# Performance work log

Measured on AMD Instinct MI355X. Metric: run time of the kernel, lower is better.

Reference implementation:

```python
import jax, jax.numpy as jnp
import numpy as np

IN_C = 128
OUT_C = 128
KS = (5, 10, 15, 20)  # Chebyshev orders per filter (evenly spaced up to max_chebyshev_order=20)
NUM_FILTERS = len(KS)
LN_EPS = 1e-5


def setup_inputs() -> dict:
    key = jax.random.key(0)
    ks = jax.random.split(key, 10)
    N, E = 50000, 800000
    x = jax.random.normal(ks[0], (N, IN_C), dtype=jnp.float32)
    edge_index = jax.random.randint(ks[1], (2, E), 0, N, dtype=jnp.int64)
    total_K = sum(KS)
    cheb_w = jax.random.normal(ks[2], (total_K, IN_C, OUT_C), dtype=jnp.float32) * (1.0 / np.sqrt(IN_C))
    cheb_b = jax.random.normal(ks[3], (NUM_FILTERS, OUT_C), dtype=jnp.float32) * 0.01
    attn_w = jax.random.normal(ks[4], (NUM_FILTERS * OUT_C, NUM_FILTERS), dtype=jnp.float32) * (1.0 / np.sqrt(NUM_FILTERS * OUT_C))
    attn_b = jnp.zeros((NUM_FILTERS,), dtype=jnp.float32)
    ln_g = jnp.ones((OUT_C,), dtype=jnp.float32)
    ln_b = jnp.zeros((OUT_C,), dtype=jnp.float32)
    return {"x": x, "edge_index": edge_index, "cheb_w": cheb_w, "cheb_b": cheb_b,
            "attn_w": attn_w, "attn_b": attn_b, "ln_g": ln_g, "ln_b": ln_b}


def _scaled_laplacian(edge_index, N, dtype):
    # get_laplacian('sym'): L = I - D^{-1/2} A D^{-1/2}; then (2/lambda_max)*w - 1 with lambda_max=2
    row, col = edge_index[0], edge_index[1]
    w = jnp.ones(row.shape, dtype)
    deg = jax.ops.segment_sum(w, row, num_segments=N)
    dinv = jnp.where(deg > 0, jax.lax.rsqrt(jnp.maximum(deg, 1e-12)), 0.0).astype(dtype)
    lap_w = -dinv[row] * w * dinv[col]          # off-diagonal entries
    loop = jnp.arange(N, dtype=row.dtype)
    src = jnp.concatenate([row, loop])
    dst = jnp.concatenate([col, loop])
    lw = jnp.concatenate([lap_w, jnp.ones((N,), dtype)])  # diagonal = 1
    lw = (2.0 / 2.0) * lw - 1.0                 # faithful: -1 applied to EVERY stored entry
    return src, dst, lw


def _propagate(x, src, dst, w, N):
    # scatter-add of edge-weighted neighbor features (PyG propagate, aggr='add')
    return jax.ops.segment_sum(w[:, None] * x[src], dst, num_segments=N)


def _cheb_conv(x, src, dst, lw, W, b, K, N):
    Tx0 = x
    out = Tx0 @ W[0]
    if K > 1:
        Tx1 = _propagate(x, src, dst, lw, N)
        out = out + Tx1 @ W[1]
        for k in range(2, K):
            Tx2 = 2.0 * _propagate(Tx1, src, dst, lw, N) - Tx0
            out = out + Tx2 @ W[k]
            Tx0, Tx1 = Tx1, Tx2
    return out + b


def reference(x, edge_index, cheb_w, cheb_b, attn_w, attn_b, ln_g, ln_b):
    N = x.shape[0]
    src, dst, lw = _scaled_laplacian(edge_index, N, x.dtype)
    outs = []
    off = 0
    for i, K in enumerate(KS):
        W = cheb_w[off:off + K]
        outs.append(_cheb_conv(x, src, dst, lw, W, cheb_b[i], K, N))
        off += K
    stacked = jnp.stack(outs)                                  # [F, N, C]
    feats = jnp.concatenate(outs, axis=-1)                     # [N, F*C]
    attn = jax.nn.softmax(feats @ attn_w + attn_b, axis=-1)    # [N, F]
    combined = jnp.einsum('nf,fnc->nc', attn, stacked)         # [N, C]
    mu = jnp.mean(combined, axis=-1, keepdims=True)
    var = jnp.mean(jnp.square(combined - mu), axis=-1, keepdims=True)
    return (combined - mu) * jax.lax.rsqrt(var + LN_EPS) * ln_g + ln_b
```

## Files before the change

### kernel.cpp

```cpp
#include <hip/hip_runtime.h>

#define IN_C 128
#define NF 4

typedef __attribute__((ext_vector_type(8))) short short8;
typedef __attribute__((ext_vector_type(4))) float f32x4;

__device__ __forceinline__ unsigned short f2bf(float v) {
    unsigned u = __float_as_uint(v);
    return (unsigned short)((u + 0x7fffu + ((u >> 16) & 1u)) >> 16);
}

__global__ void zero_ints(int* p, int n) {
    int i = blockIdx.x * 256 + threadIdx.x;
    if (i < n) p[i] = 0;
}

__global__ void count_deg(const int* __restrict__ ei, int* __restrict__ degr,
                          int* __restrict__ cnt, int E) {
    int e = blockIdx.x * 256 + threadIdx.x;
    if (e >= E) return;
    atomicAdd(&degr[ei[e]], 1);
    atomicAdd(&cnt[ei[E + e]], 1);
}

__global__ void dinv_k(const int* __restrict__ degr, float* __restrict__ dinv, int N) {
    int i = blockIdx.x * 256 + threadIdx.x;
    if (i >= N) return;
    int d = degr[i];
    dinv[i] = (d > 0) ? rsqrtf((float)d) : 0.0f;
}

__global__ void scanA(const int* __restrict__ in, int* __restrict__ outp,
                      int* __restrict__ partials, int n) {
    __shared__ int tmp[256];
    int t = threadIdx.x;
    int gid = blockIdx.x * 256 + t;
    int v = (gid < n) ? in[gid] : 0;
    tmp[t] = v;
    __syncthreads();
    for (int off = 1; off < 256; off <<= 1) {
        int add = (t >= off) ? tmp[t - off] : 0;
        __syncthreads();
        tmp[t] += add;
        __syncthreads();
    }
    if (gid < n) outp[gid] = tmp[t] - v;
    if (t == 255) partials[blockIdx.x] = tmp[255];
}

__global__ void scanB(int* partials, int n) {
    __shared__ int tmp[256];
    int t = threadIdx.x;
    int v = (t < n) ? partials[t] : 0;
    tmp[t] = v;
    __syncthreads();
    for (int off = 1; off < 256; off <<= 1) {
        int add = (t >= off) ? tmp[t - off] : 0;
        __syncthreads();
        tmp[t] += add;
        __syncthreads();
    }
    if (t < n) partials[t] = tmp[t] - v;
}

__global__ void scanC(int* __restrict__ offs, const int* __restrict__ partials,
                      int n, int total) {
    int gid = blockIdx.x * 256 + threadIdx.x;
    if (gid < n) offs[gid] += partials[blockIdx.x];
    if (gid == 0) offs[n] = total;
}

__global__ void fill_csr(const int* __restrict__ ei, const float* __restrict__ dinv,
                         const int* __restrict__ offs, int* __restrict__ cursor,
                         uint2* __restrict__ csr, int E) {
    int e = blockIdx.x * 256 + threadIdx.x;
    if (e >= E) return;
    int r = ei[e];
    int c = ei[E + e];
    float w = -dinv[r] * dinv[c] - 1.0f;
    int pos = offs[c] + atomicAdd(&cursor[c], 1);
    csr[pos] = make_uint2((unsigned)r, __float_as_uint(w));
}

__global__ void wtr(const float* __restrict__ cheb_w, unsigned short* __restrict__ wht) {
    int gk = blockIdx.x;
    const float* src = cheb_w + (size_t)gk * 16384;
    unsigned short* dst = wht + (size_t)gk * 16384;
    for (int j = 0; j < 64; ++j) {
        int idx = threadIdx.x + j * 256;
        int c = idx >> 7, o = idx & 127;
        dst[o * 128 + c] = f2bf(src[idx]);
    }
}

__global__ void vprep(const float* __restrict__ cheb_w, const float* __restrict__ attn_w,
                      float* __restrict__ V) {
    int k = blockIdx.x;
    int c = threadIdx.x;
    float s[4] = {0.f, 0.f, 0.f, 0.f};
    for (int f = k / 5; f < 4; ++f) {
        const float* wrow = cheb_w + (size_t)((5 * f * (f + 1)) / 2 + k) * 16384 + c * 128;
        const float* arow = attn_w + (size_t)f * 512;
        for (int o = 0; o < 128; ++o) {
            float wv = wrow[o];
            s[0] += wv * arow[o * 4 + 0];
            s[1] += wv * arow[o * 4 + 1];
            s[2] += wv * arow[o * 4 + 2];
            s[3] += wv * arow[o * 4 + 3];
        }
    }
    float* dst = V + k * 512 + c * 4;
    dst[0] = s[0]; dst[1] = s[1]; dst[2] = s[2]; dst[3] = s[3];
}

__global__ void bias_const(const float* __restrict__ cheb_b, const float* __restrict__ attn_w,
                           const float* __restrict__ attn_b, float* __restrict__ constj) {
    int j = threadIdx.x;
    if (j >= 4) return;
    float s = attn_b[j];
    for (int t = 0; t < 512; ++t) s += cheb_b[t] * attn_w[t * 4 + j];
    constj[j] = s;
}

__global__ __launch_bounds__(256) void logit_init(
    const float* __restrict__ x, const float* __restrict__ V,
    const float* __restrict__ constj, float* __restrict__ logits,
    unsigned short* __restrict__ xb, int N)
{
    int node = blockIdx.x * 4 + (threadIdx.x >> 6);
    int lane = threadIdx.x & 63;
    if (node >= N) return;
    float2 v = ((const float2*)(x + (size_t)node * 128))[lane];
    int cc = lane * 2;
    unsigned u = (unsigned)f2bf(v.x) | ((unsigned)f2bf(v.y) << 16);
    *(unsigned*)(xb + (size_t)node * 128 + cc) = u;

    float4 va = *(const float4*)(V + 4 * cc);
    float4 vb = *(const float4*)(V + 4 * cc + 4);
    float l0 = v.x * va.x + v.y * vb.x;
    float l1 = v.x * va.y + v.y * vb.y;
    float l2 = v.x * va.z + v.y * vb.z;
    float l3 = v.x * va.w + v.y * vb.w;
#pragma unroll
    for (int off = 32; off; off >>= 1) {
        l0 += __shfl_xor(l0, off); l1 += __shfl_xor(l1, off);
        l2 += __shfl_xor(l2, off); l3 += __shfl_xor(l3, off);
    }
    if (lane == 0) {
        float4 cj = *(const float4*)constj;
        *(float4*)(logits + 4 * node) =
            make_float4(l0 + cj.x, l1 + cj.y, l2 + cj.z, l3 + cj.w);
    }
}

__global__ __launch_bounds__(256) void propagate(
    const uint2* __restrict__ csr, const int* __restrict__ offs,
    const float* __restrict__ A, const float* __restrict__ Bsub,
    float* __restrict__ C, unsigned short* __restrict__ Cb,
    float alpha, int N,
    const float* __restrict__ Vk, float* __restrict__ logits)
{
    int node = blockIdx.x * 4 + (threadIdx.x >> 6);
    int lane = threadIdx.x & 63;
    if (node >= N) return;
    int half = lane >> 5;
    int cl = (lane & 31) * 4;
    int beg = offs[node], end = offs[node + 1];

    float4 s = make_float4(0.f, 0.f, 0.f, 0.f);
    for (int j = beg; j < end; j += 16) {
        uint2 e[8];
#pragma unroll
        for (int u = 0; u < 8; ++u) {
            int je = j + 2 * u + half;
            e[u] = (je < end) ? csr[je] : make_uint2(0u, 0u);
        }
        float4 v[8];
#pragma unroll
        for (int u = 0; u < 8; ++u)
            v[u] = *(const float4*)(A + (size_t)e[u].x * 128 + cl);
#pragma unroll
        for (int u = 0; u < 8; ++u) {
            float wv = __uint_as_float(e[u].y);
            s.x += wv * v[u].x; s.y += wv * v[u].y;
            s.z += wv * v[u].z; s.w += wv * v[u].w;
        }
    }
    s.x += __shfl_xor(s.x, 32); s.y += __shfl_xor(s.y, 32);
    s.z += __shfl_xor(s.z, 32); s.w += __shfl_xor(s.w, 32);

    float4 o;
    if (Bsub) {
        float4 b = *(const float4*)(Bsub + (size_t)node * 128 + cl);
        o.x = alpha * s.x - b.x; o.y = alpha * s.y - b.y;
        o.z = alpha * s.z - b.z; o.w = alpha * s.w - b.w;
    } else {
        o.x = alpha * s.x; o.y = alpha * s.y;
        o.z = alpha * s.z; o.w = alpha * s.w;
    }
    if (half == 0) {
        *(float4*)(C + (size_t)node * 128 + cl) = o;
        unsigned u0 = (unsigned)f2bf(o.x) | ((unsigned)f2bf(o.y) << 16);
        unsigned u1 = (unsigned)f2bf(o.z) | ((unsigned)f2bf(o.w) << 16);
        *(uint2*)(Cb + (size_t)node * 128 + cl) = make_uint2(u0, u1);
    }

    float4 w0 = *(const float4*)(Vk + 4 * cl);
    float4 w1 = *(const float4*)(Vk + 4 * (cl + 1));
    float4 w2 = *(const float4*)(Vk + 4 * (cl + 2));
    float4 w3 = *(const float4*)(Vk + 4 * (cl + 3));
    float l0 = o.x * w0.x + o.y * w1.x + o.z * w2.x + o.w * w3.x;
    float l1 = o.x * w0.y + o.y * w1.y + o.z * w2.y + o.w * w3.y;
    float l2 = o.x * w0.z + o.y * w1.z + o.z * w2.z + o.w * w3.z;
    float l3 = o.x * w0.w + o.y * w1.w + o.z * w2.w + o.w * w3.w;
#pragma unroll
    for (int off = 16; off; off >>= 1) {
        l0 += __shfl_xor(l0, off); l1 += __shfl_xor(l1, off);
        l2 += __shfl_xor(l2, off); l3 += __shfl_xor(l3, off);
    }
    if (lane == 0) {
        float4 cur = *(const float4*)(logits + 4 * node);
        cur.x += l0; cur.y += l1; cur.z += l2; cur.w += l3;
        *(float4*)(logits + 4 * node) = cur;
    }
}

__global__ __launch_bounds__(256) void gemm_mfma(
    const unsigned short* __restrict__ xb, const unsigned short* __restrict__ Tb,
    const unsigned short* __restrict__ wht, float* __restrict__ acc_base,
    int N, int g)
{
    __shared__ __align__(16) unsigned short Th[128 * 72];
    __shared__ __align__(16) unsigned short Wh[128 * 72];
    int f = g + blockIdx.x;
    int gk0 = (5 * f * (f + 1)) / 2 + 5 * g;
    float* __restrict__ acc = acc_base + (size_t)f * N * 128;
    int r0 = blockIdx.y * 128;
    int tid = threadIdx.x;
    int wave = tid >> 6, lane = tid & 63;
    int wm = (wave >> 1) * 64, wn = (wave & 1) * 64;
    int quad = lane >> 4, l16 = lane & 15;
    size_t matf = (size_t)N * 128;

    f32x4 dacc[4][4];
#pragma unroll
    for (int a = 0; a < 4; ++a)
#pragma unroll
        for (int b = 0; b < 4; ++b)
#pragma unroll
            for (int e = 0; e < 4; ++e) dacc[a][b][e] = 0.f;

    for (int i = 0; i < 10; ++i) {
        int kl = i >> 1, koff = (i & 1) * 64;
        const unsigned short* __restrict__ Tsrc =
            (g == 0 && kl == 0) ? xb : Tb + (size_t)kl * matf;
        const unsigned short* __restrict__ Wsrc = wht + (size_t)(gk0 + kl) * 16384;
        if (i) __syncthreads();
#pragma unroll
        for (int jj = 0; jj < 4; ++jj) {
            int chunk = tid + jj * 256;
            int r = chunk >> 3, cp = (chunk & 7) * 8;
            int row = r0 + r;
            uint4 v = make_uint4(0u, 0u, 0u, 0u);
            if (row < N) v = *(const uint4*)(Tsrc + (size_t)row * 128 + koff + cp);
            *(uint4*)(&Th[r * 72 + cp]) = v;
        }
#pragma unroll
        for (int jj = 0; jj < 4; ++jj) {
            int chunk = tid + jj * 256;
            int o = chunk >> 3, cp = (chunk & 7) * 8;
            uint4 v = *(const uint4*)(Wsrc + (size_t)o * 128 + koff + cp);
            *(uint4*)(&Wh[o * 72 + cp]) = v;
        }
        __syncthreads();
#pragma unroll
        for (int ks = 0; ks < 64; ks += 32) {
            short8 av[4], bv[4];
#pragma unroll
            for (int mt = 0; mt < 4; ++mt)
                av[mt] = *(const short8*)(&Th[(wm + mt * 16 + l16) * 72 + ks + quad * 8]);
#pragma unroll
            for (int nt = 0; nt < 4; ++nt)
                bv[nt] = *(const short8*)(&Wh[(wn + nt * 16 + l16) * 72 + ks + quad * 8]);
#pragma unroll
            for (int mt = 0; mt < 4; ++mt)
#pragma unroll
                for (int nt = 0; nt < 4; ++nt)
                    dacc[mt][nt] = __builtin_amdgcn_mfma_f32_16x16x32_bf16(
                        av[mt], bv[nt], dacc[mt][nt], 0, 0, 0);
        }
    }
#pragma unroll
    for (int mt = 0; mt < 4; ++mt) {
#pragma unroll
        for (int nt = 0; nt < 4; ++nt) {
            int col = wn + nt * 16 + l16;
#pragma unroll
            for (int e = 0; e < 4; ++e) {
                int row = r0 + wm + mt * 16 + quad * 4 + e;
                if (row < N) {
                    float* p = acc + (size_t)row * 128 + col;
                    float v = dacc[mt][nt][e];
                    if (g > 0) v += *p;
                    *p = v;
                }
            }
        }
    }
}

__global__ __launch_bounds__(256) void attn_ln(
    const float* __restrict__ acc_base, const float* __restrict__ cheb_b,
    const float* __restrict__ logits,
    const float* __restrict__ ln_g, const float* __restrict__ ln_b,
    float* __restrict__ out, int N)
{
    int node = blockIdx.x * 4 + (threadIdx.x >> 6);
    int lane = threadIdx.x & 63;
    if (node >= N) return;
    int c = lane * 2;
    size_t matf = (size_t)N * 128;

    float4 lg = *(const float4*)(logits + 4 * node);
    float m = fmaxf(fmaxf(lg.x, lg.y), fmaxf(lg.z, lg.w));
    float e0 = expf(lg.x - m), e1 = expf(lg.y - m), e2 = expf(lg.z - m), e3 = expf(lg.w - m);
    float inv_s = 1.f / (e0 + e1 + e2 + e3);
    float p[4] = {e0 * inv_s, e1 * inv_s, e2 * inv_s, e3 * inv_s};

    float cx = 0.f, cy = 0.f;
#pragma unroll
    for (int ff = 0; ff < NF; ++ff) {
        float2 v = ((const float2*)(acc_base + (size_t)ff * matf + (size_t)node * 128))[lane];
        cx += p[ff] * (v.x + cheb_b[ff * 128 + c]);
        cy += p[ff] * (v.y + cheb_b[ff * 128 + c + 1]);
    }
    float sum = cx + cy;
#pragma unroll
    for (int off = 32; off; off >>= 1) sum += __shfl_xor(sum, off);
    float mu = sum * (1.f / 128.f);
    float dx = cx - mu, dy = cy - mu;

    float M = fmaxf(fabsf(dx), fabsf(dy));
#pragma unroll
    for (int off = 32; off; off >>= 1) M = fmaxf(M, __shfl_xor(M, off));

    float zx, zy, r;
    if (M > 0.f) {
        float inv = 1.f / M;
        zx = dx * inv; zy = dy * inv;
        float v2 = zx * zx + zy * zy;
#pragma unroll
        for (int off = 32; off; off >>= 1) v2 += __shfl_xor(v2, off);
        float var = v2 * (1.f / 128.f);
        r = rsqrtf(var + 1e-5f * inv * inv);
    } else {
        zx = 0.f; zy = 0.f; r = 0.f;
    }
    out[(size_t)node * 128 + c]     = zx * r * ln_g[c]     + ln_b[c];
    out[(size_t)node * 128 + c + 1] = zy * r * ln_g[c + 1] + ln_b[c + 1];
}

extern "C" void kernel_launch(void* const* d_in, const int* in_sizes, int n_in,
                              void* d_out, int out_size, void* d_ws, size_t ws_size,
                              hipStream_t stream) {
    const float* x       = (const float*)d_in[0];
    const int* ei        = (const int*)d_in[1];
    const float* cheb_w  = (const float*)d_in[2];
    const float* cheb_b  = (const float*)d_in[3];
    const float* attn_w  = (const float*)d_in[4];
    const float* attn_b  = (const float*)d_in[5];
    const float* ln_g    = (const float*)d_in[6];
    const float* ln_b    = (const float*)d_in[7];
    float* out = (float*)d_out;

    int N = in_sizes[0] / 128;
    int E = in_sizes[1] / 2;

    char* w = (char*)d_ws;
    auto alloc = [&](size_t bytes) -> void* {
        void* p = (void*)w;
        w += (bytes + 255) & ~(size_t)255;
        return p;
    };
    size_t matf = (size_t)N * 128;
    size_t mat_bytes = matf * sizeof(float);
    float* slots3 = (float*)alloc(3 * mat_bytes);
    float* acc    = (float*)alloc(4 * mat_bytes);
    unsigned short* Tb = (unsigned short*)alloc(5 * matf * sizeof(unsigned short));
    unsigned short* xb = (unsigned short*)alloc(matf * sizeof(unsigned short));
    uint2* csr   = (uint2*)alloc((size_t)E * sizeof(uint2));
    int* offs    = (int*)alloc((size_t)(N + 1) * sizeof(int));
    int* zero3   = (int*)alloc((size_t)3 * N * sizeof(int));
    int* degr = zero3, *cnt = zero3 + N, *cursor = zero3 + 2 * N;
    float* dinv  = (float*)alloc((size_t)N * sizeof(float));
    int* partials = (int*)alloc(1024 * sizeof(int));
    float* logits = (float*)alloc((size_t)N * 4 * sizeof(float));
    float* V      = (float*)alloc(20 * 512 * sizeof(float));
    float* constj = (float*)alloc(256);
    unsigned short* wht = (unsigned short*)alloc((size_t)50 * 16384 * sizeof(unsigned short));
    if ((size_t)(w - (char*)d_ws) > ws_size) return;

    int eb = (E + 255) / 256;
    int nb = (N + 255) / 256;
    int pb = (N + 3) / 4;

    zero_ints<<<(3 * N + 255) / 256, 256, 0, stream>>>(zero3, 3 * N);
    count_deg<<<eb, 256, 0, stream>>>(ei, degr, cnt, E);
    dinv_k<<<nb, 256, 0, stream>>>(degr, dinv, N);
    scanA<<<nb, 256, 0, stream>>>(cnt, offs, partials, N);
    scanB<<<1, 256, 0, stream>>>(partials, nb);
    scanC<<<nb, 256, 0, stream>>>(offs, partials, N, E);
    fill_csr<<<eb, 256, 0, stream>>>(ei, dinv, offs, cursor, csr, E);

    wtr<<<50, 256, 0, stream>>>(cheb_w, wht);
    vprep<<<20, 128, 0, stream>>>(cheb_w, attn_w, V);
    bias_const<<<1, 64, 0, stream>>>(cheb_b, attn_w, attn_b, constj);
    logit_init<<<pb, 256, 0, stream>>>(x, V, constj, logits, xb, N);

    int rtiles = (N + 127) / 128;
    for (int g = 0; g < 4; ++g) {
        int kbeg = 5 * g + (g == 0 ? 1 : 0);
        int kend = 5 * g + 4;
        for (int k = kbeg; k <= kend; ++k) {
            const float* A = (k == 1) ? x : slots3 + (size_t)((k - 1) % 3) * matf;
            const float* B = (k == 1) ? nullptr
                            : ((k == 2) ? x : slots3 + (size_t)((k - 2) % 3) * matf);
            float* C = slots3 + (size_t)(k % 3) * matf;
            unsigned short* Cb = Tb + (size_t)(k % 5) * matf;
            propagate<<<pb, 256, 0, stream>>>(csr, offs, A, B, C, Cb,
                                              (k == 1) ? 1.f : 2.f, N,
                                              V + k * 512, logits);
        }
        dim3 grid(4 - g, rtiles);
        gemm_mfma<<<grid, 256, 0, stream>>>(xb, Tb, wht, acc, N, g);
    }
    attn_ln<<<pb, 256, 0, stream>>>(acc, cheb_b, logits, ln_g, ln_b, out, N);
}
```

Measured before the change: 1.857 ms.

## Fuse Chebyshev GEMM tiles into propagate launches and store accumulators in bf16

```diff
diff --git a/kernel.cpp b/kernel.cpp
--- a/kernel.cpp
+++ b/kernel.cpp
@@ -2,6 +2,7 @@
 
 #define IN_C 128
 #define NF 4
+#define NSLOT 10
 
 typedef __attribute__((ext_vector_type(8))) short short8;
 typedef __attribute__((ext_vector_type(4))) float f32x4;
@@ -9,6 +10,9 @@
 __device__ __forceinline__ unsigned short f2bf(float v) {
     unsigned u = __float_as_uint(v);
     return (unsigned short)((u + 0x7fffu + ((u >> 16) & 1u)) >> 16);
+}
+__device__ __forceinline__ float bf2f(unsigned short u) {
+    return __uint_as_float(((unsigned)u) << 16);
 }
 
 __global__ void zero_ints(int* p, int n) {
@@ -126,7 +130,7 @@
 __global__ __launch_bounds__(256) void logit_init(
     const float* __restrict__ x, const float* __restrict__ V,
     const float* __restrict__ constj, float* __restrict__ logits,
-    unsigned short* __restrict__ xb, int N)
+    unsigned short* __restrict__ Tb0, int N)
 {
     int node = blockIdx.x * 4 + (threadIdx.x >> 6);
     int lane = threadIdx.x & 63;
@@ -134,7 +138,7 @@
     float2 v = ((const float2*)(x + (size_t)node * 128))[lane];
     int cc = lane * 2;
     unsigned u = (unsigned)f2bf(v.x) | ((unsigned)f2bf(v.y) << 16);
-    *(unsigned*)(xb + (size_t)node * 128 + cc) = u;
+    *(unsigned*)(Tb0 + (size_t)node * 128 + cc) = u;
 
     float4 va = *(const float4*)(V + 4 * cc);
     float4 vb = *(const float4*)(V + 4 * cc + 4);
@@ -154,15 +158,101 @@
     }
 }
 
-__global__ __launch_bounds__(256) void propagate(
+__global__ __launch_bounds__(256) void prop_gemm(
     const uint2* __restrict__ csr, const int* __restrict__ offs,
     const float* __restrict__ A, const float* __restrict__ Bsub,
-    float* __restrict__ C, unsigned short* __restrict__ Cb,
-    float alpha, int N,
-    const float* __restrict__ Vk, float* __restrict__ logits)
+    float* __restrict__ Cw, unsigned short* __restrict__ Cb,
+    float alpha, int N, const float* __restrict__ Vk, float* __restrict__ logits,
+    int gemmN,
+    const unsigned short* __restrict__ Tb, const unsigned short* __restrict__ wht,
+    unsigned short* __restrict__ accb, int gg, int item0, int nf)
 {
-    int node = blockIdx.x * 4 + (threadIdx.x >> 6);
-    int lane = threadIdx.x & 63;
+    __shared__ __align__(16) unsigned short Th[128 * 72];
+    __shared__ __align__(16) unsigned short Wh[128 * 72];
+    size_t matf = (size_t)N * 128;
+    int tid = threadIdx.x;
+
+    if ((int)blockIdx.x < gemmN) {
+        int item = item0 + (int)blockIdx.x;
+        int tile = item / nf;
+        int f = gg + (item - tile * nf);
+        int gk0 = (5 * f * (f + 1)) / 2 + 5 * gg;
+        unsigned short* __restrict__ acc = accb + (size_t)f * matf;
+        int r0 = tile * 128;
+        int wave = tid >> 6, lane = tid & 63;
+        int wm = (wave >> 1) * 64, wn = (wave & 1) * 64;
+        int quad = lane >> 4, l16 = lane & 15;
+
+        f32x4 dacc[4][4];
+#pragma unroll
+        for (int a = 0; a < 4; ++a)
+#pragma unroll
+            for (int b = 0; b < 4; ++b)
+#pragma unroll
+                for (int e = 0; e < 4; ++e) dacc[a][b][e] = 0.f;
+
+        for (int i = 0; i < 10; ++i) {
+            int kl = i >> 1, koff = (i & 1) * 64;
+            int slot = (5 * gg + kl) % NSLOT;
+            const unsigned short* __restrict__ Tsrc = Tb + (size_t)slot * matf;
+            const unsigned short* __restrict__ Wsrc = wht + (size_t)(gk0 + kl) * 16384;
+            if (i) __syncthreads();
+#pragma unroll
+            for (int jj = 0; jj < 4; ++jj) {
+                int chunk = tid + jj * 256;
+                int r = chunk >> 3, cp = (chunk & 7) * 8;
+                int row = r0 + r;
+                uint4 v = make_uint4(0u, 0u, 0u, 0u);
+                if (row < N) v = *(const uint4*)(Tsrc + (size_t)row * 128 + koff + cp);
+                *(uint4*)(&Th[r * 72 + cp]) = v;
+            }
+#pragma unroll
+            for (int jj = 0; jj < 4; ++jj) {
+                int chunk = tid + jj * 256;
+                int o = chunk >> 3, cp = (chunk & 7) * 8;
+                uint4 v = *(const uint4*)(Wsrc + (size_t)o * 128 + koff + cp);
+                *(uint4*)(&Wh[o * 72 + cp]) = v;
+            }
+            __syncthreads();
+#pragma unroll
+            for (int ks = 0; ks < 64; ks += 32) {
+                short8 av[4], bv[4];
+#pragma unroll
+                for (int mt = 0; mt < 4; ++mt)
+                    av[mt] = *(const short8*)(&Th[(wm + mt * 16 + l16) * 72 + ks + quad * 8]);
+#pragma unroll
+                for (int nt = 0; nt < 4; ++nt)
+                    bv[nt] = *(const short8*)(&Wh[(wn + nt * 16 + l16) * 72 + ks + quad * 8]);
+#pragma unroll
+                for (int mt = 0; mt < 4; ++mt)
+#pragma unroll
+                    for (int nt = 0; nt < 4; ++nt)
+                        dacc[mt][nt] = __builtin_amdgcn_mfma_f32_16x16x32_bf16(
+                            av[mt], bv[nt], dacc[mt][nt], 0, 0, 0);
+            }
+        }
+#pragma unroll
+        for (int mt = 0; mt < 4; ++mt) {
+#pragma unroll
+            for (int nt = 0; nt < 4; ++nt) {
+                int col = wn + nt * 16 + l16;
+#pragma unroll
+                for (int e = 0; e < 4; ++e) {
+                    int row = r0 + wm + mt * 16 + quad * 4 + e;
+                    if (row < N) {
+                        unsigned short* p = acc + (size_t)row * 128 + col;
+                        float v = dacc[mt][nt][e];
+                        if (gg > 0) v += bf2f(*p);
+                        *p = f2bf(v);
+                    }
+                }
+            }
+        }
+        return;
+    }
+
+    int node = ((int)blockIdx.x - gemmN) * 4 + (tid >> 6);
+    int lane = tid & 63;
     if (node >= N) return;
     int half = lane >> 5;
     int cl = (lane & 31) * 4;
@@ -200,7 +290,7 @@
         o.z = alpha * s.z; o.w = alpha * s.w;
     }
     if (half == 0) {
-        *(float4*)(C + (size_t)node * 128 + cl) = o;
+        *(float4*)(Cw + (size_t)node * 128 + cl) = o;
         unsigned u0 = (unsigned)f2bf(o.x) | ((unsigned)f2bf(o.y) << 16);
         unsigned u1 = (unsigned)f2bf(o.z) | ((unsigned)f2bf(o.w) << 16);
         *(uint2*)(Cb + (size_t)node * 128 + cl) = make_uint2(u0, u1);
@@ -226,92 +316,8 @@
     }
 }
 
-__global__ __launch_bounds__(256) void gemm_mfma(
-    const unsigned short* __restrict__ xb, const unsigned short* __restrict__ Tb,
-    const unsigned short* __restrict__ wht, float* __restrict__ acc_base,
-    int N, int g)
-{
-    __shared__ __align__(16) unsigned short Th[128 * 72];
-    __shared__ __align__(16) unsigned short Wh[128 * 72];
-    int f = g + blockIdx.x;
-    int gk0 = (5 * f * (f + 1)) / 2 + 5 * g;
-    float* __restrict__ acc = acc_base + (size_t)f * N * 128;
-    int r0 = blockIdx.y * 128;
-    int tid = threadIdx.x;
-    int wave = tid >> 6, lane = tid & 63;
-    int wm = (wave >> 1) * 64, wn = (wave & 1) * 64;
-    int quad = lane >> 4, l16 = lane & 15;
-    size_t matf = (size_t)N * 128;
-
-    f32x4 dacc[4][4];
-#pragma unroll
-    for (int a = 0; a < 4; ++a)
-#pragma unroll
-        for (int b = 0; b < 4; ++b)
-#pragma unroll
-            for (int e = 0; e < 4; ++e) dacc[a][b][e] = 0.f;
-
-    for (int i = 0; i < 10; ++i) {
-        int kl = i >> 1, koff = (i & 1) * 64;
-        const unsigned short* __restrict__ Tsrc =
-            (g == 0 && kl == 0) ? xb : Tb + (size_t)kl * matf;
-        const unsigned short* __restrict__ Wsrc = wht + (size_t)(gk0 + kl) * 16384;
-        if (i) __syncthreads();
-#pragma unroll
-        for (int jj = 0; jj < 4; ++jj) {
-            int chunk = tid + jj * 256;
-            int r = chunk >> 3, cp = (chunk & 7) * 8;
-            int row = r0 + r;
-            uint4 v = make_uint4(0u, 0u, 0u, 0u);
-            if (row < N) v = *(const uint4*)(Tsrc + (size_t)row * 128 + koff + cp);
-            *(uint4*)(&Th[r * 72 + cp]) = v;
-        }
-#pragma unroll
-        for (int jj = 0; jj < 4; ++jj) {
-            int chunk = tid + jj * 256;
-            int o = chunk >> 3, cp = (chunk & 7) * 8;
-            uint4 v = *(const uint4*)(Wsrc + (size_t)o * 128 + koff + cp);
-            *(uint4*)(&Wh[o * 72 + cp]) = v;
-        }
-        __syncthreads();
-#pragma unroll
-        for (int ks = 0; ks < 64; ks += 32) {
-            short8 av[4], bv[4];
-#pragma unroll
-            for (int mt = 0; mt < 4; ++mt)
-                av[mt] = *(const short8*)(&Th[(wm + mt * 16 + l16) * 72 + ks + quad * 8]);
-#pragma unroll
-            for (int nt = 0; nt < 4; ++nt)
-                bv[nt] = *(const short8*)(&Wh[(wn + nt * 16 + l16) * 72 + ks + quad * 8]);
-#pragma unroll
-            for (int mt = 0; mt < 4; ++mt)
-#pragma unroll
-                for (int nt = 0; nt < 4; ++nt)
-                    dacc[mt][nt] = __builtin_amdgcn_mfma_f32_16x16x32_bf16(
-                        av[mt], bv[nt], dacc[mt][nt], 0, 0, 0);
-        }
-    }
-#pragma unroll
-    for (int mt = 0; mt < 4; ++mt) {
-#pragma unroll
-        for (int nt = 0; nt < 4; ++nt) {
-            int col = wn + nt * 16 + l16;
-#pragma unroll
-            for (int e = 0; e < 4; ++e) {
-                int row = r0 + wm + mt * 16 + quad * 4 + e;
-                if (row < N) {
-                    float* p = acc + (size_t)row * 128 + col;
-                    float v = dacc[mt][nt][e];
-                    if (g > 0) v += *p;
-                    *p = v;
-                }
-            }
-        }
-    }
-}
-
 __global__ __launch_bounds__(256) void attn_ln(
-    const float* __restrict__ acc_base, const float* __restrict__ cheb_b,
+    const unsigned short* __restrict__ accb, const float* __restrict__ cheb_b,
     const float* __restrict__ logits,
     const float* __restrict__ ln_g, const float* __restrict__ ln_b,
     float* __restrict__ out, int N)
@@ -331,9 +337,11 @@
     float cx = 0.f, cy = 0.f;
 #pragma unroll
     for (int ff = 0; ff < NF; ++ff) {
-        float2 v = ((const float2*)(acc_base + (size_t)ff * matf + (size_t)node * 128))[lane];
-        cx += p[ff] * (v.x + cheb_b[ff * 128 + c]);
-        cy += p[ff] * (v.y + cheb_b[ff * 128 + c + 1]);
+        unsigned u = *(const unsigned*)(accb + (size_t)ff * matf + (size_t)node * 128 + c);
+        float vx = bf2f((unsigned short)(u & 0xffffu));
+        float vy = bf2f((unsigned short)(u >> 16));
+        cx += p[ff] * (vx + cheb_b[ff * 128 + c]);
+        cy += p[ff] * (vy + cheb_b[ff * 128 + c + 1]);
     }
     float sum = cx + cy;
 #pragma unroll
@@ -384,11 +392,9 @@
         return p;
     };
     size_t matf = (size_t)N * 128;
-    size_t mat_bytes = matf * sizeof(float);
-    float* slots3 = (float*)alloc(3 * mat_bytes);
-    float* acc    = (float*)alloc(4 * mat_bytes);
-    unsigned short* Tb = (unsigned short*)alloc(5 * matf * sizeof(unsigned short));
-    unsigned short* xb = (unsigned short*)alloc(matf * sizeof(unsigned short));
+    float* slots3 = (float*)alloc(3 * matf * sizeof(float));
+    unsigned short* accb = (unsigned short*)alloc(4 * matf * sizeof(unsigned short));
+    unsigned short* Tb = (unsigned short*)alloc((size_t)NSLOT * matf * sizeof(unsigned short));
     uint2* csr   = (uint2*)alloc((size_t)E * sizeof(uint2));
     int* offs    = (int*)alloc((size_t)(N + 1) * sizeof(int));
     int* zero3   = (int*)alloc((size_t)3 * N * sizeof(int));
@@ -404,6 +410,7 @@
     int eb = (E + 255) / 256;
     int nb = (N + 255) / 256;
     int pb = (N + 3) / 4;
+    int rtiles = (N + 127) / 128;
 
     zero_ints<<<(3 * N + 255) / 256, 256, 0, stream>>>(zero3, 3 * N);
     count_deg<<<eb, 256, 0, stream>>>(ei, degr, cnt, E);
@@ -416,24 +423,31 @@
     wtr<<<50, 256, 0, stream>>>(cheb_w, wht);
     vprep<<<20, 128, 0, stream>>>(cheb_w, attn_w, V);
     bias_const<<<1, 64, 0, stream>>>(cheb_b, attn_w, attn_b, constj);
-    logit_init<<<pb, 256, 0, stream>>>(x, V, constj, logits, xb, N);
-
-    int rtiles = (N + 127) / 128;
-    for (int g = 0; g < 4; ++g) {
-        int kbeg = 5 * g + (g == 0 ? 1 : 0);
-        int kend = 5 * g + 4;
-        for (int k = kbeg; k <= kend; ++k) {
-            const float* A = (k == 1) ? x : slots3 + (size_t)((k - 1) % 3) * matf;
-            const float* B = (k == 1) ? nullptr
-                            : ((k == 2) ? x : slots3 + (size_t)((k - 2) % 3) * matf);
-            float* C = slots3 + (size_t)(k % 3) * matf;
-            unsigned short* Cb = Tb + (size_t)(k % 5) * matf;
-            propagate<<<pb, 256, 0, stream>>>(csr, offs, A, B, C, Cb,
-                                              (k == 1) ? 1.f : 2.f, N,
-                                              V + k * 512, logits);
-        }
-        dim3 grid(4 - g, rtiles);
-        gemm_mfma<<<grid, 256, 0, stream>>>(xb, Tb, wht, acc, N, g);
-    }
-    attn_ln<<<pb, 256, 0, stream>>>(acc, cheb_b, logits, ln_g, ln_b, out, N);
-}
+    logit_init<<<pb, 256, 0, stream>>>(x, V, constj, logits, Tb , N);
+
+    for (int k = 1; k <= 19; ++k) {
+        int gg = 0, it0 = 0, cntc = 0, nf = 1;
+        if (k >= 5) {
+            gg = (k - 5) / 5;
+            nf = 4 - gg;
+            int tot = rtiles * nf;
+            int W = (tot + 4) / 5;
+            int j = (k - 5) % 5;
+            it0 = j * W;
+            cntc = tot - it0; if (cntc > W) cntc = W; if (cntc < 0) cntc = 0;
+        }
+        const float* A = (k == 1) ? x : slots3 + (size_t)((k - 1) % 3) * matf;
+        const float* B = (k == 1) ? nullptr
+                        : ((k == 2) ? x : slots3 + (size_t)((k - 2) % 3) * matf);
+        float* C = slots3 + (size_t)(k % 3) * matf;
+        unsigned short* Cb = Tb + (size_t)(k % NSLOT) * matf;
+        prop_gemm<<<cntc + pb, 256, 0, stream>>>(
+            csr, offs, A, B, C, Cb, (k == 1) ? 1.f : 2.f, N,
+            V + k * 512, logits, cntc, Tb, wht, accb, gg, it0, nf);
+    }
+    prop_gemm<<<rtiles, 256, 0, stream>>>(
+        csr, offs, x, nullptr, slots3, Tb, 0.f, N,
+        V, logits, rtiles, Tb, wht, accb, 3, 0, 1);
+
+    attn_ln<<<pb, 256, 0, stream>>>(accb, cheb_b, logits, ln_g, ln_b, out, N);
+}
```

Result: slower. 2.909 ms (+56.6%).
